# Optimization experiments

Measured on AMD Instinct MI355X. Metric: run time of the kernel, lower is better.

## Reference

```python
import jax, jax.numpy as jnp
import numpy as np

N = 65536    # cluster nodes
E = 1048576  # edges (~avg degree 16); first N are self-loops (asserted in original)
B = 32       # graphs in the batch
D = 64       # channels (hard-coded 64 in source)
NL = 4       # 4 stacked PointTransformerConv encoders
NC = 2       # classes (Linear(64, 2) in source)


def _mlp2(y, W1, b1, W2, b2):
    # PyG MLP(plain_last=False) in eval mode: Linear -> BN(identity at init) -> ReLU, twice
    return jax.nn.relu(jax.nn.relu(y @ W1 + b1) @ W2 + b2)


def _seg_softmax(a, dst, n):
    # channelwise softmax over incoming edges of each destination node
    m = jax.ops.segment_max(a, dst, num_segments=n)
    e = jnp.exp(a - m[dst])
    s = jax.ops.segment_sum(e, dst, num_segments=n)
    return e / s[dst]


def _pt_conv(x, pos, src, dst, Wl, Ws, Wd, pW1, pb1, pW2, pb2, aW1, ab1, aW2, ab2):
    # PyG PointTransformerConv (add_self_loops=False, default sum aggregation)
    n = x.shape[0]
    v = x @ Wl      # lin   -> value, gathered at src (x_j)
    a_s = x @ Ws    # lin_src -> alpha_j
    a_d = x @ Wd    # lin_dst -> alpha_i
    delta = _mlp2(pos[dst] - pos[src], pW1, pb1, pW2, pb2)            # pos_nn(pos_i - pos_j), [E, D]
    alpha = _mlp2(a_d[dst] - a_s[src] + delta, aW1, ab1, aW2, ab2)    # attn_nn(...), [E, D]
    alpha = _seg_softmax(alpha, dst, n)
    msg = alpha * (v[src] + delta)                                     # [E, D]
    return jax.ops.segment_sum(msg, dst, num_segments=n)               # [N, D]


def setup_inputs() -> dict:
    key = jax.random.key(0)
    ks = jax.random.split(key, 16)
    x = jax.random.normal(ks[0], (N, D), dtype=jnp.float32)
    pos = jax.random.uniform(ks[1], (N, 2), dtype=jnp.float32)
    src = jax.random.randint(ks[2], (E,), 0, N)
    dst = jax.random.randint(ks[3], (E,), 0, N)
    loops = jnp.arange(N)
    src = src.at[:N].set(loops)  # guarantee self-loops
    dst = dst.at[:N].set(loops)
    edge_index = jnp.stack([src, dst]).astype(jnp.int32)
    batch = ((jnp.arange(N) * B) // N).astype(jnp.int32)  # sorted graph ids, every graph non-empty
    s = jnp.float32(0.05)
    def rn(k, shape):
        return jax.random.normal(k, shape, dtype=jnp.float32) * s
    return {
        'x': x, 'pos': pos,
        'W_lin': rn(ks[4], (NL, D, D)),
        'W_src': rn(ks[5], (NL, D, D)),
        'W_dst': rn(ks[6], (NL, D, D)),
        'pos_W1': rn(ks[7], (NL, 2, D)),
        'pos_b1': jnp.zeros((NL, D), jnp.float32),
        'pos_W2': rn(ks[8], (NL, D, D)),
        'pos_b2': jnp.zeros((NL, D), jnp.float32),
        'attn_W1': rn(ks[9], (NL, D, D)),
        'attn_b1': jnp.zeros((NL, D), jnp.float32),
        'attn_W2': rn(ks[10], (NL, D, D)),
        'attn_b2': jnp.zeros((NL, D), jnp.float32),
        'out_W': rn(ks[11], (D, NC)),
        'out_b': jnp.zeros((NC,), jnp.float32),
        'edge_index': edge_index,
        'batch': batch,
    }


def reference(x, pos, W_lin, W_src, W_dst, pos_W1, pos_b1, pos_W2, pos_b2,
              attn_W1, attn_b1, attn_W2, attn_b2, out_W, out_b, edge_index, batch):
    src, dst = edge_index[0], edge_index[1]
    h = x
    for i in range(NL):  # 4 stacked cluster encoders (fixed layer count)
        h = _pt_conv(h, pos, src, dst, W_lin[i], W_src[i], W_dst[i],
                     pos_W1[i], pos_b1[i], pos_W2[i], pos_b2[i],
                     attn_W1[i], attn_b1[i], attn_W2[i], attn_b2[i])
    g = jax.ops.segment_max(h, batch, num_segments=B)  # global_max_pool -> [B, D]
    return g @ out_W + out_b                           # [B, NC]
```

## Files before the change

kernel.cpp:

```cpp
#include <hip/hip_runtime.h>
#include <hip/hip_bf16.h>
#include <math.h>

#define N_NODES 65536
#define N_EDGES 1048576
#define NB      32
#define D       64
#define NLAYERS 4
#define G       16
#define CH      32
#define AST     72
#define PST     68

typedef __attribute__((ext_vector_type(8))) short short8;
typedef __attribute__((ext_vector_type(4))) float f32x4;

__device__ __forceinline__ float relu_f(float x){ return x > 0.f ? x : 0.f; }
__device__ __forceinline__ unsigned short bfbits(float x){
    __bf16 h = (__bf16)x;
    return __builtin_bit_cast(unsigned short, h);
}
__device__ __forceinline__ float bfval(float x){
    __bf16 h = (__bf16)x;
    return (float)h;
}
__device__ __forceinline__ f32x4 mfma16(short8 a, short8 b, f32x4 c){
    return __builtin_amdgcn_mfma_f32_16x16x32_bf16(a, b, c, 0, 0, 0);
}


__global__ void k_zero(int* __restrict__ p){
    p[blockIdx.x * 256 + threadIdx.x] = 0;
}

__global__ void k_hist(const int* __restrict__ dst, int* __restrict__ deg){
    int e = blockIdx.x * 256 + threadIdx.x;
    if (e < N_EDGES) atomicAdd(&deg[dst[e]], 1);
}

__global__ void k_scan1(const int* __restrict__ deg, int* __restrict__ part, int* __restrict__ bsum){
    __shared__ int s[256];
    int t = threadIdx.x;
    int i = blockIdx.x * 256 + t;
    int v = deg[i];
    s[t] = v; __syncthreads();
    for (int ofs = 1; ofs < 256; ofs <<= 1){
        int tv = (t >= ofs) ? s[t - ofs] : 0;
        __syncthreads();
        s[t] += tv;
        __syncthreads();
    }
    part[i] = s[t] - v;
    if (t == 255) bsum[blockIdx.x] = s[255];
}

__global__ void k_scan2(const int* __restrict__ bsum, int* __restrict__ bofs){
    __shared__ int s[256];
    int t = threadIdx.x;
    int v = bsum[t];
    s[t] = v; __syncthreads();
    for (int ofs = 1; ofs < 256; ofs <<= 1){
        int tv = (t >= ofs) ? s[t - ofs] : 0;
        __syncthreads();
        s[t] += tv;
        __syncthreads();
    }
    bofs[t] = s[t] - v;
}

__global__ void k_scan3(const int* __restrict__ part, const int* __restrict__ bofs,
                        int* __restrict__ off, int* __restrict__ cursor){
    int i = blockIdx.x * 256 + threadIdx.x;
    int o = part[i] + bofs[i >> 8];
    off[i] = o; cursor[i] = o;
    if (i == 0) off[N_NODES] = N_EDGES;
}

__global__ void k_scatter(const int* __restrict__ ei, const float* __restrict__ pos,
                          int* __restrict__ cursor, int* __restrict__ srcs,
                          float* __restrict__ pdb){
    int e = blockIdx.x * 256 + threadIdx.x;
    if (e >= N_EDGES) return;
    int s = ei[e], d = ei[N_EDGES + e];
    int p = atomicAdd(&cursor[d], 1);
    srcs[p]    = s;
    pdb[2*p]   = pos[2*d]   - pos[2*s];
    pdb[2*p+1] = pos[2*d+1] - pos[2*s+1];
}


__global__ void k_pack(const float* __restrict__ pW2, const float* __restrict__ aW1,
                       const float* __restrict__ aW2, unsigned short* __restrict__ bpk){
    int b  = blockIdx.x;
    int kf = b & 1, nb = (b >> 1) & 3;
    int mat = (b >> 3) % 3, L = b / 24;
    int t = threadIdx.x;
    int lane = t & 63, jj = (t >> 6) * 2;
    const float* W = (mat == 0 ? pW2 : (mat == 1 ? aW1 : aW2)) + (size_t)L * D * D;
    int n = nb * 16 + (lane & 15);
    unsigned short* dsthi = bpk + (size_t)L * 24576
                          + (((size_t)mat * 4 + nb) * 2 + kf) * 512 + lane * 8 + jj;
    #pragma unroll
    for (int u = 0; u < 2; ++u){
        int j = jj + u;
        int k = kf * 32 + (lane >> 4) * 8 + j;
        float w = W[k * D + n];
        float hv = bfval(w);
        dsthi[u]         = bfbits(w);
        dsthi[12288 + u] = bfbits(w - hv);
    }
}


__global__ __launch_bounds__(256) void k_nodegemm(
    const float* __restrict__ h,
    const float* __restrict__ Wl, const float* __restrict__ Ws, const float* __restrict__ Wd,
    float* __restrict__ v, float* __restrict__ as_, float* __restrict__ ad)
{
    __shared__ float HT[D * 68];
    int row0 = blockIdx.x * 64;
    int t = threadIdx.x;
    {
        int r  = t >> 2;
        int kb = (t & 3) * 16;
        const float4* hp = (const float4*)(h + (size_t)(row0 + r) * D + kb);
        #pragma unroll
        for (int i4 = 0; i4 < 4; ++i4){
            float4 a = hp[i4];
            HT[(kb + i4*4 + 0)*68 + r] = a.x;
            HT[(kb + i4*4 + 1)*68 + r] = a.y;
            HT[(kb + i4*4 + 2)*68 + r] = a.z;
            HT[(kb + i4*4 + 3)*68 + r] = a.w;
        }
    }
    __syncthreads();
    int tr = t >> 4, tc = t & 15;
    int r0 = tr * 4, c0 = tc * 4;
    float accl[4][4] = {}, accs[4][4] = {}, accd[4][4] = {};
    #pragma unroll 8
    for (int k = 0; k < D; ++k){
        float4 a  = *(const float4*)&HT[k*68 + r0];
        float4 bl = *(const float4*)(Wl + k*D + c0);
        float4 bs = *(const float4*)(Ws + k*D + c0);
        float4 bd = *(const float4*)(Wd + k*D + c0);
        float av[4] = {a.x, a.y, a.z, a.w};
        #pragma unroll
        for (int i = 0; i < 4; ++i){
            accl[i][0] += av[i]*bl.x; accl[i][1] += av[i]*bl.y;
            accl[i][2] += av[i]*bl.z; accl[i][3] += av[i]*bl.w;
            accs[i][0] += av[i]*bs.x; accs[i][1] += av[i]*bs.y;
            accs[i][2] += av[i]*bs.z; accs[i][3] += av[i]*bs.w;
            accd[i][0] += av[i]*bd.x; accd[i][1] += av[i]*bd.y;
            accd[i][2] += av[i]*bd.z; accd[i][3] += av[i]*bd.w;
        }
    }
    #pragma unroll
    for (int i = 0; i < 4; ++i){
        size_t o = (size_t)(row0 + r0 + i) * D + c0;
        *(float4*)(v  + o) = make_float4(accl[i][0], accl[i][1], accl[i][2], accl[i][3]);
        *(float4*)(as_+ o) = make_float4(accs[i][0], accs[i][1], accs[i][2], accs[i][3]);
        *(float4*)(ad + o) = make_float4(accd[i][0], accd[i][1], accd[i][2], accd[i][3]);
    }
}


__device__ __forceinline__ void load_bfrag(const unsigned short* __restrict__ bpk,
                                           int g, int w, int lane,
                                           short8& Bh0, short8& Bh1,
                                           short8& Bl0, short8& Bl1)
{
    int bo = ((g*4 + w)*2)*512 + lane*8;
    asm volatile("" : "+v"(bo));
    Bh0 = __builtin_bit_cast(short8, *(const uint4*)(bpk + bo));
    Bh1 = __builtin_bit_cast(short8, *(const uint4*)(bpk + bo + 512));
    Bl0 = __builtin_bit_cast(short8, *(const uint4*)(bpk + 12288 + bo));
    Bl1 = __builtin_bit_cast(short8, *(const uint4*)(bpk + 12288 + bo + 512));
}

__device__ __forceinline__ void gemm_tile2(const unsigned short* __restrict__ Ah,
                                           const unsigned short* __restrict__ Al,
                                           short8 Bh0, short8 Bh1, short8 Bl0, short8 Bl1,
                                           int ln, int q, f32x4* accs)
{
    #pragma unroll
    for (int mt = 0; mt < 2; ++mt){
        int ro = (mt*16 + ln) * AST;
        short8 ah0 = __builtin_bit_cast(short8, *(const uint4*)(Ah + ro + q*8));
        short8 ah1 = __builtin_bit_cast(short8, *(const uint4*)(Ah + ro + 32 + q*8));
        short8 al0 = __builtin_bit_cast(short8, *(const uint4*)(Al + ro + q*8));
        short8 al1 = __builtin_bit_cast(short8, *(const uint4*)(Al + ro + 32 + q*8));
        f32x4 acc = {0.f, 0.f, 0.f, 0.f};
        acc = mfma16(ah0, Bh0, acc);
        acc = mfma16(ah1, Bh1, acc);
        acc = mfma16(al0, Bh0, acc);
        acc = mfma16(al1, Bh1, acc);
        acc = mfma16(ah0, Bl0, acc);
        acc = mfma16(ah1, Bl1, acc);
        accs[mt] = acc;
    }
}

__global__ __launch_bounds__(256) void k_edge(
    const int* __restrict__ off, const int* __restrict__ srcs, const float* __restrict__ pdb,
    const float* __restrict__ v, const float* __restrict__ as_, const float* __restrict__ ad,
    const float* __restrict__ pW1, const float* __restrict__ pb1, const float* __restrict__ pb2,
    const float* __restrict__ ab1, const float* __restrict__ ab2,
    const unsigned short* __restrict__ bpk,
    float* __restrict__ hout)
{
    __shared__ __align__(16) unsigned short ALDS[2 * CH * AST];
    __shared__ __align__(16) unsigned short ULDS[2 * CH * AST];
    __shared__ int s_sp[CH];
    __shared__ int s_off[20];

    unsigned short* Ahi = ALDS;
    unsigned short* Alo = ALDS + CH * AST;
    unsigned short* Uhi = ULDS;
    unsigned short* Ulo = ULDS + CH * AST;
    float* Pf  = (float*)ULDS;
    float* PMf = (float*)ALDS;

    int t  = threadIdx.x;
    int n0 = blockIdx.x * G;
    if (t <= G) s_off[t] = off[n0 + t];
    __syncthreads();
    int e_begin = s_off[0], e_end = s_off[G];

    int w = t >> 6, lane = t & 63;
    int q = lane >> 4, ln = lane & 15;
    int c = w * 16 + ln;

    float pb2c = pb2[c], ab1c = ab1[c], ab2c = ab2[c];

    float den[4] = {0.f, 0.f, 0.f, 0.f};
    float num[4] = {0.f, 0.f, 0.f, 0.f};

    for (int ec = e_begin; ec < e_end; ec += CH){
        int cnt = min(CH, e_end - ec);
        {
            int e8 = t >> 3, kb = (t & 7) * 8;
            int g = ec + ((e8 < cnt) ? e8 : 0);
            if (t < CH){
                int gg = ec + ((t < cnt) ? t : 0);
                int s = srcs[gg];
                int l = 0;
                while (l < G-1 && gg >= s_off[l+1]) ++l;
                s_sp[t] = s | (l << 16);
            }
            float2 pd = *(const float2*)(pdb + 2*g);
            float p0 = pd.x, p1 = pd.y;
            unsigned int hw[4], lw[4];
            #pragma unroll
            for (int i2 = 0; i2 < 4; ++i2){
                int k = kb + i2*2;
                float f0 = relu_f(fmaf(p1, pW1[D + k],     fmaf(p0, pW1[k],     pb1[k])));
                float f1 = relu_f(fmaf(p1, pW1[D + k + 1], fmaf(p0, pW1[k + 1], pb1[k + 1])));
                unsigned short h0 = bfbits(f0), h1 = bfbits(f1);
                float r0f = f0 - bfval(f0), r1f = f1 - bfval(f1);
                unsigned short l0 = bfbits(r0f), l1 = bfbits(r1f);
                hw[i2] = (unsigned int)h0 | ((unsigned int)h1 << 16);
                lw[i2] = (unsigned int)l0 | ((unsigned int)l1 << 16);
            }
            *(uint4*)&Ahi[e8*AST + kb] = make_uint4(hw[0], hw[1], hw[2], hw[3]);
            *(uint4*)&Alo[e8*AST + kb] = make_uint4(lw[0], lw[1], lw[2], lw[3]);
        }
        __syncthreads();
        float Mreg[8];
        {
            short8 Bh0, Bh1, Bl0, Bl1;
            load_bfrag(bpk, 0, w, lane, Bh0, Bh1, Bl0, Bl1);
            float pa[8], pvd[8];
            #pragma unroll
            for (int mt = 0; mt < 2; ++mt)
                #pragma unroll
                for (int r = 0; r < 4; ++r){
                    int i = mt*4 + r;
                    int e = mt*16 + q*4 + r;
                    int sp = s_sp[e];
                    int s  = sp & 0xFFFF;
                    int dn = n0 + (sp >> 16);
                    Mreg[i] = v  [(size_t)s * D + c];
                    pa[i]   = as_[(size_t)s * D + c];
                    pvd[i]  = ad [(size_t)dn * D + c];
                }
            f32x4 accs[2];
            gemm_tile2(Ahi, Alo, Bh0, Bh1, Bl0, Bl1, ln, q, accs);
            #pragma unroll
            for (int mt = 0; mt < 2; ++mt){
                #pragma unroll
                for (int r = 0; r < 4; ++r){
                    int i = mt*4 + r;
                    int e = mt*16 + q*4 + r;
                    float dlt = relu_f(accs[mt][r] + pb2c);
                    float uu = pvd[i] - pa[i] + dlt;
                    Mreg[i] += dlt;
                    Uhi[e*AST + c] = bfbits(uu);
                    Ulo[e*AST + c] = bfbits(uu - bfval(uu));
                }
            }
        }
        __syncthreads();
        {
            short8 Bh0, Bh1, Bl0, Bl1;
            load_bfrag(bpk, 1, w, lane, Bh0, Bh1, Bl0, Bl1);
            f32x4 accs[2];
            gemm_tile2(Uhi, Ulo, Bh0, Bh1, Bl0, Bl1, ln, q, accs);
            #pragma unroll
            for (int mt = 0; mt < 2; ++mt){
                #pragma unroll
                for (int r = 0; r < 4; ++r){
                    int e = mt*16 + q*4 + r;
                    float t2 = relu_f(accs[mt][r] + ab1c);
                    Ahi[e*AST + c] = bfbits(t2);
                    Alo[e*AST + c] = bfbits(t2 - bfval(t2));
                }
            }
        }
        __syncthreads();
        {
            short8 Bh0, Bh1, Bl0, Bl1;
            load_bfrag(bpk, 2, w, lane, Bh0, Bh1, Bl0, Bl1);
            f32x4 accs[2];
            gemm_tile2(Ahi, Alo, Bh0, Bh1, Bl0, Bl1, ln, q, accs);
            #pragma unroll
            for (int mt = 0; mt < 2; ++mt){
                #pragma unroll
                for (int r = 0; r < 4; ++r){
                    int e = mt*16 + q*4 + r;
                    float a = relu_f(accs[mt][r] + ab2c);
                    float p = __expf(a);
                    accs[mt][r] = p;
                    Pf[e*PST + c] = p;
                }
            }
            __syncthreads();
            #pragma unroll
            for (int mt = 0; mt < 2; ++mt){
                #pragma unroll
                for (int r = 0; r < 4; ++r){
                    int e = mt*16 + q*4 + r;
                    PMf[e*PST + c] = accs[mt][r] * Mreg[mt*4 + r];
                }
            }
        }
        __syncthreads();
        #pragma unroll
        for (int qn = 0; qn < 4; ++qn){
            int l  = w*4 + qn;
            int gs = max(s_off[l], ec);
            int ge = min(s_off[l+1], ec + cnt);
            float dd = den[qn], nn = num[qn];
            for (int g = gs; g < ge; ++g){
                int e = g - ec;
                dd += Pf [e*PST + lane];
                nn += PMf[e*PST + lane];
            }
            den[qn] = dd; num[qn] = nn;
        }
        __syncthreads();
    }
    #pragma unroll
    for (int qn = 0; qn < 4; ++qn){
        int n = n0 + w*4 + qn;
        hout[(size_t)n * D + lane] = num[qn] / den[qn];
    }
}


__global__ __launch_bounds__(256) void k_pool(const float* __restrict__ h,
                                              const float* __restrict__ outW,
                                              const float* __restrict__ outb,
                                              float* __restrict__ out)
{
    __shared__ float sm[4][64];
    __shared__ float sp[2][64];
    int b = blockIdx.x;
    int t = threadIdx.x, j = t & 63, g = t >> 6;
    float mx = -1e30f;
    for (int r = b*2048 + g; r < (b+1)*2048; r += 4)
        mx = fmaxf(mx, h[(size_t)r * D + j]);
    sm[g][j] = mx;
    __syncthreads();
    if (t < 64){
        float m = fmaxf(fmaxf(sm[0][j], sm[1][j]), fmaxf(sm[2][j], sm[3][j]));
        sp[0][j] = m * outW[j*2 + 0];
        sp[1][j] = m * outW[j*2 + 1];
    }
    __syncthreads();
    if (t == 0){
        float s0 = outb[0], s1 = outb[1];
        for (int k = 0; k < 64; ++k){ s0 += sp[0][k]; s1 += sp[1][k]; }
        out[b*2]   = s0;
        out[b*2+1] = s1;
    }
}


extern "C" void kernel_launch(void* const* d_in, const int* in_sizes, int n_in,
                              void* d_out, int out_size, void* d_ws, size_t ws_size,
                              hipStream_t stream)
{
    const float* x    = (const float*)d_in[0];
    const float* pos  = (const float*)d_in[1];
    const float* Wl   = (const float*)d_in[2];
    const float* Ws   = (const float*)d_in[3];
    const float* Wd   = (const float*)d_in[4];
    const float* pW1  = (const float*)d_in[5];
    const float* pb1  = (const float*)d_in[6];
    const float* pW2  = (const float*)d_in[7];
    const float* pb2  = (const float*)d_in[8];
    const float* aW1  = (const float*)d_in[9];
    const float* ab1  = (const float*)d_in[10];
    const float* aW2  = (const float*)d_in[11];
    const float* ab2  = (const float*)d_in[12];
    const float* outW = (const float*)d_in[13];
    const float* outb = (const float*)d_in[14];
    const int*   ei   = (const int*)d_in[15];
    float* out = (float*)d_out;

    char* wp = (char*)d_ws;
    auto alloc = [&](size_t bytes){
        void* p = (void*)wp;
        wp += (bytes + 255) & ~(size_t)255;
        return p;
    };
    int*   deg    = (int*)  alloc((size_t)N_NODES * 4);
    int*   part   = (int*)  alloc((size_t)N_NODES * 4);
    int*   bsum   = (int*)  alloc(1024);
    int*   bofs   = (int*)  alloc(1024);
    int*   off    = (int*)  alloc((size_t)(N_NODES + 1) * 4);
    int*   cursor = (int*)  alloc((size_t)N_NODES * 4);
    int*   srcs   = (int*)  alloc((size_t)N_EDGES * 4);
    float* pdb    = (float*)alloc((size_t)N_EDGES * 8);
    float* vv     = (float*)alloc((size_t)N_NODES * D * 4);
    float* as_    = (float*)alloc((size_t)N_NODES * D * 4);
    float* ad     = (float*)alloc((size_t)N_NODES * D * 4);
    float* h0     = (float*)alloc((size_t)N_NODES * D * 4);
    float* h1     = (float*)alloc((size_t)N_NODES * D * 4);
    unsigned short* bpk = (unsigned short*)alloc((size_t)NLAYERS * 24576 * 2);

    k_zero   <<<256,  256, 0, stream>>>(deg);
    k_hist   <<<4096, 256, 0, stream>>>(ei + N_EDGES, deg);
    k_scan1  <<<256,  256, 0, stream>>>(deg, part, bsum);
    k_scan2  <<<1,    256, 0, stream>>>(bsum, bofs);
    k_scan3  <<<256,  256, 0, stream>>>(part, bofs, off, cursor);
    k_scatter<<<4096, 256, 0, stream>>>(ei, pos, cursor, srcs, pdb);
    k_pack   <<<96,   256, 0, stream>>>(pW2, aW1, aW2, bpk);

    const float* hin = x;
    float* hbuf[2] = { h0, h1 };
    for (int L = 0; L < NLAYERS; ++L){
        float* hout = hbuf[L & 1];
        k_nodegemm<<<N_NODES/64, 256, 0, stream>>>(hin,
            Wl + (size_t)L*D*D, Ws + (size_t)L*D*D, Wd + (size_t)L*D*D,
            vv, as_, ad);
        k_edge<<<N_NODES/G, 256, 0, stream>>>(off, srcs, pdb, vv, as_, ad,
            pW1 + (size_t)L*2*D, pb1 + (size_t)L*D, pb2 + (size_t)L*D,
            ab1 + (size_t)L*D, ab2 + (size_t)L*D,
            bpk + (size_t)L*24576,
            hout);
        hin = hout;
    }
    k_pool<<<NB, 256, 0, stream>>>(hin, outW, outb, out);
}
```

Baseline: 1.506 ms.

## Give each wave its own four nodes and drop block-wide barriers in edge kernel

Each 64-lane wave now processes the edges of its own 4 destination nodes in 16-edge chunks. It computes all 64 output channels through four MFMA column blocks, and each wave has private LDS tiles. This removes every per-chunk __syncthreads and the coupling between waves that have different edge counts. The first MLP layer now reads its weights as float4. The code relies on lanes of one wave seeing each other's LDS writes without an explicit barrier, and it holds more registers per thread (16-entry Mreg/pa arrays and four accumulators), which may lower occupancy.

```diff
diff --git a/kernel.cpp b/kernel.cpp
--- a/kernel.cpp
+++ b/kernel.cpp
@@ -8,7 +8,7 @@
 #define D       64
 #define NLAYERS 4
 #define G       16
-#define CH      32
+#define EC      16
 #define AST     72
 #define PST     68
 
@@ -165,11 +165,11 @@
 
 
 __device__ __forceinline__ void load_bfrag(const unsigned short* __restrict__ bpk,
-                                           int g, int w, int lane,
+                                           int g, int nb, int lane,
                                            short8& Bh0, short8& Bh1,
                                            short8& Bl0, short8& Bl1)
 {
-    int bo = ((g*4 + w)*2)*512 + lane*8;
+    int bo = ((g*4 + nb)*2)*512 + lane*8;
     asm volatile("" : "+v"(bo));
     Bh0 = __builtin_bit_cast(short8, *(const uint4*)(bpk + bo));
     Bh1 = __builtin_bit_cast(short8, *(const uint4*)(bpk + bo + 512));
@@ -177,27 +177,17 @@
     Bl1 = __builtin_bit_cast(short8, *(const uint4*)(bpk + 12288 + bo + 512));
 }
 
-__device__ __forceinline__ void gemm_tile2(const unsigned short* __restrict__ Ah,
-                                           const unsigned short* __restrict__ Al,
-                                           short8 Bh0, short8 Bh1, short8 Bl0, short8 Bl1,
-                                           int ln, int q, f32x4* accs)
-{
-    #pragma unroll
-    for (int mt = 0; mt < 2; ++mt){
-        int ro = (mt*16 + ln) * AST;
-        short8 ah0 = __builtin_bit_cast(short8, *(const uint4*)(Ah + ro + q*8));
-        short8 ah1 = __builtin_bit_cast(short8, *(const uint4*)(Ah + ro + 32 + q*8));
-        short8 al0 = __builtin_bit_cast(short8, *(const uint4*)(Al + ro + q*8));
-        short8 al1 = __builtin_bit_cast(short8, *(const uint4*)(Al + ro + 32 + q*8));
-        f32x4 acc = {0.f, 0.f, 0.f, 0.f};
-        acc = mfma16(ah0, Bh0, acc);
-        acc = mfma16(ah1, Bh1, acc);
-        acc = mfma16(al0, Bh0, acc);
-        acc = mfma16(al1, Bh1, acc);
-        acc = mfma16(ah0, Bl0, acc);
-        acc = mfma16(ah1, Bl1, acc);
-        accs[mt] = acc;
-    }
+__device__ __forceinline__ f32x4 gemm6(short8 ah0, short8 ah1, short8 al0, short8 al1,
+                                       short8 Bh0, short8 Bh1, short8 Bl0, short8 Bl1)
+{
+    f32x4 acc = {0.f, 0.f, 0.f, 0.f};
+    acc = mfma16(ah0, Bh0, acc);
+    acc = mfma16(ah1, Bh1, acc);
+    acc = mfma16(al0, Bh0, acc);
+    acc = mfma16(al1, Bh1, acc);
+    acc = mfma16(ah0, Bl0, acc);
+    acc = mfma16(ah1, Bl1, acc);
+    return acc;
 }
 
 __global__ __launch_bounds__(256) void k_edge(
@@ -208,142 +198,165 @@
     const unsigned short* __restrict__ bpk,
     float* __restrict__ hout)
 {
-    __shared__ __align__(16) unsigned short ALDS[2 * CH * AST];
-    __shared__ __align__(16) unsigned short ULDS[2 * CH * AST];
-    __shared__ int s_sp[CH];
+    __shared__ __align__(16) unsigned short ALDS[4 * 2 * EC * AST];
+    __shared__ __align__(16) unsigned short ULDS[4 * 2 * EC * AST];
+    __shared__ int s_sp[4 * EC];
     __shared__ int s_off[20];
-
-    unsigned short* Ahi = ALDS;
-    unsigned short* Alo = ALDS + CH * AST;
-    unsigned short* Uhi = ULDS;
-    unsigned short* Ulo = ULDS + CH * AST;
-    float* Pf  = (float*)ULDS;
-    float* PMf = (float*)ALDS;
 
     int t  = threadIdx.x;
     int n0 = blockIdx.x * G;
     if (t <= G) s_off[t] = off[n0 + t];
     __syncthreads();
-    int e_begin = s_off[0], e_end = s_off[G];
 
     int w = t >> 6, lane = t & 63;
     int q = lane >> 4, ln = lane & 15;
-    int c = w * 16 + ln;
-
-    float pb2c = pb2[c], ab1c = ab1[c], ab2c = ab2[c];
+
+    unsigned short* Thi = ALDS + w * (2 * EC * AST);
+    unsigned short* Tlo = Thi + EC * AST;
+    unsigned short* Uhi = ULDS + w * (2 * EC * AST);
+    unsigned short* Ulo = Uhi + EC * AST;
+    float* Pf  = (float*)Uhi;
+    float* PMf = (float*)Thi;
+    int*   spw = s_sp + w * EC;
+
+    int e_begin = s_off[w*4], e_end = s_off[w*4 + 4];
+
+    float pb2c[4], ab1c[4], ab2c[4];
+    #pragma unroll
+    for (int nb = 0; nb < 4; ++nb){
+        pb2c[nb] = pb2[nb*16 + ln];
+        ab1c[nb] = ab1[nb*16 + ln];
+        ab2c[nb] = ab2[nb*16 + ln];
+    }
 
     float den[4] = {0.f, 0.f, 0.f, 0.f};
     float num[4] = {0.f, 0.f, 0.f, 0.f};
 
-    for (int ec = e_begin; ec < e_end; ec += CH){
-        int cnt = min(CH, e_end - ec);
+    for (int ec = e_begin; ec < e_end; ec += EC){
+        int cnt = min(EC, e_end - ec);
         {
-            int e8 = t >> 3, kb = (t & 7) * 8;
-            int g = ec + ((e8 < cnt) ? e8 : 0);
-            if (t < CH){
-                int gg = ec + ((t < cnt) ? t : 0);
+            if (lane < EC){
+                int gg = ec + ((lane < cnt) ? lane : 0);
                 int s = srcs[gg];
                 int l = 0;
-                while (l < G-1 && gg >= s_off[l+1]) ++l;
-                s_sp[t] = s | (l << 16);
-            }
+                while (l < 3 && gg >= s_off[w*4 + l + 1]) ++l;
+                spw[lane] = s | (l << 16);
+            }
+            int e8 = lane >> 2, kb = (lane & 3) * 16;
+            int g = ec + ((e8 < cnt) ? e8 : 0);
             float2 pd = *(const float2*)(pdb + 2*g);
             float p0 = pd.x, p1 = pd.y;
-            unsigned int hw[4], lw[4];
-            #pragma unroll
-            for (int i2 = 0; i2 < 4; ++i2){
-                int k = kb + i2*2;
-                float f0 = relu_f(fmaf(p1, pW1[D + k],     fmaf(p0, pW1[k],     pb1[k])));
-                float f1 = relu_f(fmaf(p1, pW1[D + k + 1], fmaf(p0, pW1[k + 1], pb1[k + 1])));
-                unsigned short h0 = bfbits(f0), h1 = bfbits(f1);
-                float r0f = f0 - bfval(f0), r1f = f1 - bfval(f1);
-                unsigned short l0 = bfbits(r0f), l1 = bfbits(r1f);
-                hw[i2] = (unsigned int)h0 | ((unsigned int)h1 << 16);
-                lw[i2] = (unsigned int)l0 | ((unsigned int)l1 << 16);
-            }
-            *(uint4*)&Ahi[e8*AST + kb] = make_uint4(hw[0], hw[1], hw[2], hw[3]);
-            *(uint4*)&Alo[e8*AST + kb] = make_uint4(lw[0], lw[1], lw[2], lw[3]);
-        }
-        __syncthreads();
-        float Mreg[8];
+            unsigned int hw[8], lw[8];
+            #pragma unroll
+            for (int i4 = 0; i4 < 4; ++i4){
+                float4 wa = *(const float4*)(pW1 + kb + i4*4);
+                float4 wb = *(const float4*)(pW1 + D + kb + i4*4);
+                float4 bb = *(const float4*)(pb1 + kb + i4*4);
+                float f0 = relu_f(fmaf(p1, wb.x, fmaf(p0, wa.x, bb.x)));
+                float f1 = relu_f(fmaf(p1, wb.y, fmaf(p0, wa.y, bb.y)));
+                float f2 = relu_f(fmaf(p1, wb.z, fmaf(p0, wa.z, bb.z)));
+                float f3 = relu_f(fmaf(p1, wb.w, fmaf(p0, wa.w, bb.w)));
+                hw[i4*2]   = (unsigned int)bfbits(f0) | ((unsigned int)bfbits(f1) << 16);
+                hw[i4*2+1] = (unsigned int)bfbits(f2) | ((unsigned int)bfbits(f3) << 16);
+                lw[i4*2]   = (unsigned int)bfbits(f0 - bfval(f0)) | ((unsigned int)bfbits(f1 - bfval(f1)) << 16);
+                lw[i4*2+1] = (unsigned int)bfbits(f2 - bfval(f2)) | ((unsigned int)bfbits(f3 - bfval(f3)) << 16);
+            }
+            *(uint4*)&Thi[e8*AST + kb]     = make_uint4(hw[0], hw[1], hw[2], hw[3]);
+            *(uint4*)&Thi[e8*AST + kb + 8] = make_uint4(hw[4], hw[5], hw[6], hw[7]);
+            *(uint4*)&Tlo[e8*AST + kb]     = make_uint4(lw[0], lw[1], lw[2], lw[3]);
+            *(uint4*)&Tlo[e8*AST + kb + 8] = make_uint4(lw[4], lw[5], lw[6], lw[7]);
+        }
+        float Mreg[16];
         {
-            short8 Bh0, Bh1, Bl0, Bl1;
-            load_bfrag(bpk, 0, w, lane, Bh0, Bh1, Bl0, Bl1);
-            float pa[8], pvd[8];
-            #pragma unroll
-            for (int mt = 0; mt < 2; ++mt)
+            int sv[4], dl[4];
+            #pragma unroll
+            for (int r = 0; r < 4; ++r){
+                int sp = spw[q*4 + r];
+                sv[r] = sp & 0xFFFF;
+                dl[r] = sp >> 16;
+            }
+            float pa[16];
+            #pragma unroll
+            for (int nb = 0; nb < 4; ++nb)
                 #pragma unroll
                 for (int r = 0; r < 4; ++r){
-                    int i = mt*4 + r;
-                    int e = mt*16 + q*4 + r;
-                    int sp = s_sp[e];
-                    int s  = sp & 0xFFFF;
-                    int dn = n0 + (sp >> 16);
-                    Mreg[i] = v  [(size_t)s * D + c];
-                    pa[i]   = as_[(size_t)s * D + c];
-                    pvd[i]  = ad [(size_t)dn * D + c];
+                    int c = nb*16 + ln;
+                    Mreg[nb*4 + r] = v  [(size_t)sv[r] * D + c];
+                    pa  [nb*4 + r] = as_[(size_t)sv[r] * D + c];
                 }
-            f32x4 accs[2];
-            gemm_tile2(Ahi, Alo, Bh0, Bh1, Bl0, Bl1, ln, q, accs);
-            #pragma unroll
-            for (int mt = 0; mt < 2; ++mt){
+            int ro = ln * AST;
+            short8 ah0 = __builtin_bit_cast(short8, *(const uint4*)(Thi + ro + q*8));
+            short8 ah1 = __builtin_bit_cast(short8, *(const uint4*)(Thi + ro + 32 + q*8));
+            short8 al0 = __builtin_bit_cast(short8, *(const uint4*)(Tlo + ro + q*8));
+            short8 al1 = __builtin_bit_cast(short8, *(const uint4*)(Tlo + ro + 32 + q*8));
+            f32x4 acc[4];
+            #pragma unroll
+            for (int nb = 0; nb < 4; ++nb){
+                short8 Bh0, Bh1, Bl0, Bl1;
+                load_bfrag(bpk, 0, nb, lane, Bh0, Bh1, Bl0, Bl1);
+                acc[nb] = gemm6(ah0, ah1, al0, al1, Bh0, Bh1, Bl0, Bl1);
+            }
+            #pragma unroll
+            for (int nb = 0; nb < 4; ++nb)
                 #pragma unroll
                 for (int r = 0; r < 4; ++r){
-                    int i = mt*4 + r;
-                    int e = mt*16 + q*4 + r;
-                    float dlt = relu_f(accs[mt][r] + pb2c);
-                    float uu = pvd[i] - pa[i] + dlt;
+                    int i = nb*4 + r, e = q*4 + r, c = nb*16 + ln;
+                    float dlt = relu_f(acc[nb][r] + pb2c[nb]);
+                    int dn = n0 + w*4 + dl[r];
+                    float vd = ad[(size_t)dn * D + c];
+                    float uu = vd - pa[i] + dlt;
                     Mreg[i] += dlt;
                     Uhi[e*AST + c] = bfbits(uu);
                     Ulo[e*AST + c] = bfbits(uu - bfval(uu));
                 }
-            }
-        }
-        __syncthreads();
+        }
         {
-            short8 Bh0, Bh1, Bl0, Bl1;
-            load_bfrag(bpk, 1, w, lane, Bh0, Bh1, Bl0, Bl1);
-            f32x4 accs[2];
-            gemm_tile2(Uhi, Ulo, Bh0, Bh1, Bl0, Bl1, ln, q, accs);
-            #pragma unroll
-            for (int mt = 0; mt < 2; ++mt){
+            int ro = ln * AST;
+            short8 ah0 = __builtin_bit_cast(short8, *(const uint4*)(Uhi + ro + q*8));
+            short8 ah1 = __builtin_bit_cast(short8, *(const uint4*)(Uhi + ro + 32 + q*8));
+            short8 al0 = __builtin_bit_cast(short8, *(const uint4*)(Ulo + ro + q*8));
+            short8 al1 = __builtin_bit_cast(short8, *(const uint4*)(Ulo + ro + 32 + q*8));
+            f32x4 acc[4];
+            #pragma unroll
+            for (int nb = 0; nb < 4; ++nb){
+                short8 Bh0, Bh1, Bl0, Bl1;
+                load_bfrag(bpk, 1, nb, lane, Bh0, Bh1, Bl0, Bl1);
+                acc[nb] = gemm6(ah0, ah1, al0, al1, Bh0, Bh1, Bl0, Bl1);
+            }
+            #pragma unroll
+            for (int nb = 0; nb < 4; ++nb)
                 #pragma unroll
                 for (int r = 0; r < 4; ++r){
-                    int e = mt*16 + q*4 + r;
-                    float t2 = relu_f(accs[mt][r] + ab1c);
-                    Ahi[e*AST + c] = bfbits(t2);
-                    Alo[e*AST + c] = bfbits(t2 - bfval(t2));
+                    int e = q*4 + r, c = nb*16 + ln;
+                    float t2 = relu_f(acc[nb][r] + ab1c[nb]);
+                    Thi[e*AST + c] = bfbits(t2);
+                    Tlo[e*AST + c] = bfbits(t2 - bfval(t2));
                 }
-            }
-        }
-        __syncthreads();
+        }
         {
-            short8 Bh0, Bh1, Bl0, Bl1;
-            load_bfrag(bpk, 2, w, lane, Bh0, Bh1, Bl0, Bl1);
-            f32x4 accs[2];
-            gemm_tile2(Ahi, Alo, Bh0, Bh1, Bl0, Bl1, ln, q, accs);
-            #pragma unroll
-            for (int mt = 0; mt < 2; ++mt){
+            int ro = ln * AST;
+            short8 ah0 = __builtin_bit_cast(short8, *(const uint4*)(Thi + ro + q*8));
+            short8 ah1 = __builtin_bit_cast(short8, *(const uint4*)(Thi + ro + 32 + q*8));
+            short8 al0 = __builtin_bit_cast(short8, *(const uint4*)(Tlo + ro + q*8));
+            short8 al1 = __builtin_bit_cast(short8, *(const uint4*)(Tlo + ro + 32 + q*8));
+            f32x4 acc[4];
+            #pragma unroll
+            for (int nb = 0; nb < 4; ++nb){
+                short8 Bh0, Bh1, Bl0, Bl1;
+                load_bfrag(bpk, 2, nb, lane, Bh0, Bh1, Bl0, Bl1);
+                acc[nb] = gemm6(ah0, ah1, al0, al1, Bh0, Bh1, Bl0, Bl1);
+            }
+            #pragma unroll
+            for (int nb = 0; nb < 4; ++nb)
                 #pragma unroll
                 for (int r = 0; r < 4; ++r){
-                    int e = mt*16 + q*4 + r;
-                    float a = relu_f(accs[mt][r] + ab2c);
+                    int e = q*4 + r, c = nb*16 + ln;
+                    float a = relu_f(acc[nb][r] + ab2c[nb]);
                     float p = __expf(a);
-                    accs[mt][r] = p;
-                    Pf[e*PST + c] = p;
+                    Pf [e*PST + c] = p;
+                    PMf[e*PST + c] = p * Mreg[nb*4 + r];
                 }
-            }
-            __syncthreads();
-            #pragma unroll
-            for (int mt = 0; mt < 2; ++mt){
-                #pragma unroll
-                for (int r = 0; r < 4; ++r){
-                    int e = mt*16 + q*4 + r;
-                    PMf[e*PST + c] = accs[mt][r] * Mreg[mt*4 + r];
-                }
-            }
-        }
-        __syncthreads();
+        }
         #pragma unroll
         for (int qn = 0; qn < 4; ++qn){
             int l  = w*4 + qn;
@@ -357,7 +370,6 @@
             }
             den[qn] = dd; num[qn] = nn;
         }
-        __syncthreads();
     }
     #pragma unroll
     for (int qn = 0; qn < 4; ++qn){
```

Result: slower. 1.604 ms (+6.5%).
